# Performance work log

Hardware: AMD Instinct MI355X
Metric: run time of the kernel (lower is better)

The kernel has to match this reference:

```python
import jax, jax.numpy as jnp
import numpy as np
from jax import lax

K = 5          # pooling window (kernel_size=5, padding=2)
PAD = 2
NEG_SLOPE = 0.01  # LeakyReLU default


def _avg_pool5(x):
    # count_include_pad=True (torch default): zero-pad then divide by K
    s = lax.reduce_window(x, 0.0, lax.add, (1, 1, K), (1, 1, 1),
                          ((0, 0), (0, 0), (PAD, PAD)))
    return s / K


def _max_pool5(x):
    return lax.reduce_window(x, -jnp.inf, lax.max, (1, 1, K), (1, 1, 1),
                             ((0, 0), (0, 0), (PAD, PAD)))


def setup_inputs() -> dict:
    key = jax.random.key(0)
    k1, k2, k3 = jax.random.split(key, 3)
    B, C, T = 32, 128, 4096
    x = jax.random.normal(k1, (B, C, T), dtype=jnp.float32)
    conv_weight = jax.random.normal(k2, (C, 1, 6, K), dtype=jnp.float32) * 0.1
    conv_bias = jax.random.normal(k3, (C,), dtype=jnp.float32) * 0.1
    return {"x": x, "conv_weight": conv_weight, "conv_bias": conv_bias}


def reference(x, conv_weight, conv_bias):
    B, C, T = x.shape
    g_mean = jnp.broadcast_to(jnp.mean(x, axis=2, keepdims=True), (B, C, T))
    avg_x = _avg_pool5(x)
    avg_x2 = _avg_pool5(x * x)
    rolling_var = jnp.maximum(avg_x2 - avg_x * avg_x, 1e-6)
    rolling_std = jnp.sqrt(rolling_var)
    third_moment = (x - avg_x) ** 3
    rolling_max = _max_pool5(x)
    rolling_min = -_max_pool5(-x)
    # dropout is identity in eval mode
    gen_in = jnp.stack([x, g_mean, rolling_std, third_moment,
                        rolling_max, rolling_min], axis=2)  # [B,C,6,T]
    out = lax.conv_general_dilated(
        gen_in, conv_weight,
        window_strides=(1, 1),
        padding=((0, 0), (PAD, PAD)),
        dimension_numbers=("NCHW", "OIHW", "NCHW"),
        feature_group_count=C)  # [B,C,1,T]
    out = out + conv_bias[None, :, None, None]
    out = out[:, :, :, :T]
    out = jnp.where(out > 0, out, NEG_SLOPE * out)  # LeakyReLU
    out = jnp.squeeze(out, axis=2)  # [B,C,T]
    return jnp.transpose(x + out, (0, 2, 1))  # [B,T,C]
```

## Files before the change

### kernel.cpp

```cpp
#include <hip/hip_runtime.h>
#include <math.h>

#define T_LEN 4096
#define C_CH  128
#define B_N   32

__global__ __launch_bounds__(256) void row_mean_kernel(const float* __restrict__ x,
                                                       float* __restrict__ means) {
    const int wid  = ((blockIdx.x << 8) + threadIdx.x) >> 6;
    const int lane = threadIdx.x & 63;
    const float4* r = (const float4*)(x + ((size_t)wid << 12));
    float s = 0.f;
    #pragma unroll
    for (int i = 0; i < 16; ++i) {
        float4 v = r[lane + (i << 6)];
        s += (v.x + v.y) + (v.z + v.w);
    }
    #pragma unroll
    for (int off = 32; off > 0; off >>= 1) s += __shfl_down(s, off, 64);
    if (lane == 0) means[wid] = s * (1.0f / T_LEN);
}

#define LT 16
#define TT 64

__global__ __launch_bounds__(256, 4) void fused_kernel(const float* __restrict__ x,
                                                       const float* __restrict__ w,
                                                       const float* __restrict__ bias,
                                                       const float* __restrict__ means,
                                                       float* __restrict__ out) {
    const int b    = blockIdx.z;
    const int cblk = blockIdx.y;
    const int tblk = blockIdx.x;
    const int tid  = threadIdx.x;
    const int c    = cblk * 64 + (tid & 63);
    const int th   = tid >> 6;
    const int ts   = tblk * TT + th * LT;

    const float* xr  = x + ((size_t)(b * C_CH + c)) * T_LEN;
    const float mean = means[b * C_CH + c];
    const float bs   = bias[c];

    float2 wv2[15];
    const float2* pw2 = (const float2*)(w + c * 30);
    #pragma unroll
    for (int i = 0; i < 15; ++i) wv2[i] = pw2[i];
    #define W(idx) (((idx) & 1) ? wv2[(idx) >> 1].y : wv2[(idx) >> 1].x)

    const int gbase = ts - 8;
    float* po = out + ((size_t)(b * T_LEN + ts)) * C_CH + c;

    if (gbase >= 0 && gbase + 32 <= T_LEN) {
        float va[32];
        const float4* p = (const float4*)(xr + gbase);
        #pragma unroll
        for (int i = 0; i < 8; ++i) {
            float4 v = p[i];
            va[4*i+0] = v.x; va[4*i+1] = v.y; va[4*i+2] = v.z; va[4*i+3] = v.w;
        }

        const float w1s = ((W(5) + W(6)) + (W(7) + W(8))) + W(9);
        float acc[LT];
        #pragma unroll
        for (int i = 0; i < LT; ++i) acc[i] = fmaf(mean, w1s, bs);

        #pragma unroll
        for (int lj = 0; lj < LT + 4; ++lj) {
            const float v0 = va[lj+4], v1 = va[lj+5], v2 = va[lj+6], v3 = va[lj+7], v4 = va[lj+8];
            const float s  = ((v0 + v1) + (v2 + v3)) + v4;
            float s2 = v0 * v0;
            s2 = fmaf(v1, v1, s2); s2 = fmaf(v2, v2, s2);
            s2 = fmaf(v3, v3, s2); s2 = fmaf(v4, v4, s2);
            const float mx = fmaxf(fmaxf(fmaxf(v0, v1), fmaxf(v2, v3)), v4);
            const float mn = fminf(fminf(fminf(v0, v1), fminf(v2, v3)), v4);
            const float avg = s * 0.2f;
            float var = fmaf(-avg, avg, s2 * 0.2f);
            var = fmaxf(var, 1e-6f);
            const float sd = __builtin_amdgcn_sqrtf(var);
            const float dm = v2 - avg;
            const float tm = dm * dm * dm;

            #pragma unroll
            for (int dt = -2; dt <= 2; ++dt) {
                const int lt = lj - 2 + dt;
                if (lt < 0 || lt >= LT) continue;
                const int k = 2 - dt;
                float a = acc[lt];
                a = fmaf(v2, W(k),      a);
                a = fmaf(sd, W(10 + k), a);
                a = fmaf(tm, W(15 + k), a);
                a = fmaf(mx, W(20 + k), a);
                a = fmaf(mn, W(25 + k), a);
                acc[lt] = a;
            }
        }

        #pragma unroll
        for (int lt = 0; lt < LT; ++lt) {
            float o = acc[lt];
            o = fmaxf(o, 0.01f * o);
            po[lt * C_CH] = va[lt + 8] + o;
        }
    } else {
        float va[32];
        #pragma unroll
        for (int i = 0; i < 32; ++i) {
            int g = gbase + i;
            va[i] = (g >= 0 && g < T_LEN) ? xr[g] : 0.f;
        }
        float acc[LT];
        #pragma unroll
        for (int i = 0; i < LT; ++i) acc[i] = bs;

        #pragma unroll
        for (int lj = 0; lj < LT + 4; ++lj) {
            const int j = ts - 2 + lj;
            if (j < 0 || j >= T_LEN) continue;
            float s = 0.f, s2 = 0.f, mx = -INFINITY, mn = INFINITY;
            #pragma unroll
            for (int d = -2; d <= 2; ++d) {
                int gk = j + d;
                if (gk >= 0 && gk < T_LEN) {
                    float v = va[lj + 6 + d];
                    s += v; s2 = fmaf(v, v, s2);
                    mx = fmaxf(mx, v); mn = fminf(mn, v);
                }
            }
            const float avg = s * 0.2f;
            float var = fmaf(-avg, avg, s2 * 0.2f);
            var = fmaxf(var, 1e-6f);
            const float sd = __builtin_amdgcn_sqrtf(var);
            const float xc = va[lj + 6];
            const float dm = xc - avg;
            const float tm = dm * dm * dm;

            #pragma unroll
            for (int dt = -2; dt <= 2; ++dt) {
                const int lt = lj - 2 + dt;
                if (lt < 0 || lt >= LT) continue;
                const int k = 2 - dt;
                float a = acc[lt];
                a = fmaf(xc,   W(k),      a);
                a = fmaf(mean, W(5 + k),  a);
                a = fmaf(sd,   W(10 + k), a);
                a = fmaf(tm,   W(15 + k), a);
                a = fmaf(mx,   W(20 + k), a);
                a = fmaf(mn,   W(25 + k), a);
                acc[lt] = a;
            }
        }

        #pragma unroll
        for (int lt = 0; lt < LT; ++lt) {
            float o = acc[lt];
            o = fmaxf(o, 0.01f * o);
            po[lt * C_CH] = va[lt + 8] + o;
        }
    }
    #undef W
}

extern "C" void kernel_launch(void* const* d_in, const int* in_sizes, int n_in,
                              void* d_out, int out_size, void* d_ws, size_t ws_size,
                              hipStream_t stream) {
    const float* x    = (const float*)d_in[0];
    const float* w    = (const float*)d_in[1];
    const float* bias = (const float*)d_in[2];
    float* means = (float*)d_ws;
    float* out   = (float*)d_out;

    row_mean_kernel<<<dim3((B_N * C_CH) / 4), dim3(256), 0, stream>>>(x, means);
    fused_kernel<<<dim3(T_LEN / TT, C_CH / 64, B_N), dim3(256), 0, stream>>>(x, w, bias, means, out);
}
```

Before: 139.0 us.

## Stage x tile with halo in LDS via cooperative float4 loads and transpose

```diff
diff --git a/kernel.cpp b/kernel.cpp
--- a/kernel.cpp
+++ b/kernel.cpp
@@ -4,6 +4,11 @@
 #define T_LEN 4096
 #define C_CH  128
 #define B_N   32
+#define LT 16
+#define TT 64
+#define NT_BLK (T_LEN / TT)
+#define HALO 80
+#define LSTR 65
 
 __global__ __launch_bounds__(256) void row_mean_kernel(const float* __restrict__ x,
                                                        float* __restrict__ means) {
@@ -21,23 +26,44 @@
     if (lane == 0) means[wid] = s * (1.0f / T_LEN);
 }
 
-#define LT 16
-#define TT 64
-
 __global__ __launch_bounds__(256, 4) void fused_kernel(const float* __restrict__ x,
                                                        const float* __restrict__ w,
                                                        const float* __restrict__ bias,
                                                        const float* __restrict__ means,
                                                        float* __restrict__ out) {
+    __shared__ float lds[HALO * LSTR];
     const int b    = blockIdx.z;
     const int cblk = blockIdx.y;
     const int tblk = blockIdx.x;
     const int tid  = threadIdx.x;
-    const int c    = cblk * 64 + (tid & 63);
-    const int th   = tid >> 6;
-    const int ts   = tblk * TT + th * LT;
+    const int T0   = tblk * TT;
+    const float* xc0 = x + ((size_t)b * C_CH + cblk * 64) * T_LEN;
 
-    const float* xr  = x + ((size_t)(b * C_CH + c)) * T_LEN;
+    const bool edge = (tblk == 0) || (tblk == NT_BLK - 1);
+
+    #pragma unroll
+    for (int k = 0; k < 5; ++k) {
+        const int j  = tid + (k << 8);
+        const int r  = j / 20;
+        const int q  = j - r * 20;
+        const int tg = T0 - 8 + (q << 2);
+        float4 v;
+        if (!edge || ((unsigned)tg < (unsigned)T_LEN)) {
+            v = *(const float4*)(xc0 + (size_t)r * T_LEN + tg);
+        } else {
+            v.x = 0.f; v.y = 0.f; v.z = 0.f; v.w = 0.f;
+        }
+        float* dst = &lds[(size_t)(tg - (T0 - 8)) * LSTR + r];
+        dst[0 * LSTR] = v.x; dst[1 * LSTR] = v.y;
+        dst[2 * LSTR] = v.z; dst[3 * LSTR] = v.w;
+    }
+    __syncthreads();
+
+    const int ci = tid & 63;
+    const int th = tid >> 6;
+    const int c  = cblk * 64 + ci;
+    const int ts = T0 + th * LT;
+
     const float mean = means[b * C_CH + c];
     const float bs   = bias[c];
 
@@ -47,18 +73,16 @@
     for (int i = 0; i < 15; ++i) wv2[i] = pw2[i];
     #define W(idx) (((idx) & 1) ? wv2[(idx) >> 1].y : wv2[(idx) >> 1].x)
 
-    const int gbase = ts - 8;
+    float va[32];
+    {
+        const float* src = &lds[(size_t)(th * LT) * LSTR + ci];
+        #pragma unroll
+        for (int i = 0; i < 32; ++i) va[i] = src[i * LSTR];
+    }
+
     float* po = out + ((size_t)(b * T_LEN + ts)) * C_CH + c;
 
-    if (gbase >= 0 && gbase + 32 <= T_LEN) {
-        float va[32];
-        const float4* p = (const float4*)(xr + gbase);
-        #pragma unroll
-        for (int i = 0; i < 8; ++i) {
-            float4 v = p[i];
-            va[4*i+0] = v.x; va[4*i+1] = v.y; va[4*i+2] = v.z; va[4*i+3] = v.w;
-        }
-
+    if (!edge) {
         const float w1s = ((W(5) + W(6)) + (W(7) + W(8))) + W(9);
         float acc[LT];
         #pragma unroll
@@ -102,12 +126,6 @@
             po[lt * C_CH] = va[lt + 8] + o;
         }
     } else {
-        float va[32];
-        #pragma unroll
-        for (int i = 0; i < 32; ++i) {
-            int g = gbase + i;
-            va[i] = (g >= 0 && g < T_LEN) ? xr[g] : 0.f;
-        }
         float acc[LT];
         #pragma unroll
         for (int i = 0; i < LT; ++i) acc[i] = bs;
@@ -170,5 +188,5 @@
     float* out   = (float*)d_out;
 
     row_mean_kernel<<<dim3((B_N * C_CH) / 4), dim3(256), 0, stream>>>(x, means);
-    fused_kernel<<<dim3(T_LEN / TT, C_CH / 64, B_N), dim3(256), 0, stream>>>(x, w, bias, means, out);
+    fused_kernel<<<dim3(NT_BLK, C_CH / 64, B_N), dim3(256), 0, stream>>>(x, w, bias, means, out);
 }
```

New measurement: 190.8 us. 37.3% more time.

## Process four time tiles per block with register prefetch of next window

Applied to the files above, without the earlier changes.

```diff
diff --git a/kernel.cpp b/kernel.cpp
--- a/kernel.cpp
+++ b/kernel.cpp
@@ -4,6 +4,10 @@
 #define T_LEN 4096
 #define C_CH  128
 #define B_N   32
+#define LT 16
+#define TT 64
+#define TILES 4
+#define NT_BLK (T_LEN / (TT * TILES))
 
 __global__ __launch_bounds__(256) void row_mean_kernel(const float* __restrict__ x,
                                                        float* __restrict__ means) {
@@ -21,44 +25,12 @@
     if (lane == 0) means[wid] = s * (1.0f / T_LEN);
 }
 
-#define LT 16
-#define TT 64
-
-__global__ __launch_bounds__(256, 4) void fused_kernel(const float* __restrict__ x,
-                                                       const float* __restrict__ w,
-                                                       const float* __restrict__ bias,
-                                                       const float* __restrict__ means,
-                                                       float* __restrict__ out) {
-    const int b    = blockIdx.z;
-    const int cblk = blockIdx.y;
-    const int tblk = blockIdx.x;
-    const int tid  = threadIdx.x;
-    const int c    = cblk * 64 + (tid & 63);
-    const int th   = tid >> 6;
-    const int ts   = tblk * TT + th * LT;
-
-    const float* xr  = x + ((size_t)(b * C_CH + c)) * T_LEN;
-    const float mean = means[b * C_CH + c];
-    const float bs   = bias[c];
-
-    float2 wv2[15];
-    const float2* pw2 = (const float2*)(w + c * 30);
-    #pragma unroll
-    for (int i = 0; i < 15; ++i) wv2[i] = pw2[i];
-    #define W(idx) (((idx) & 1) ? wv2[(idx) >> 1].y : wv2[(idx) >> 1].x)
-
-    const int gbase = ts - 8;
-    float* po = out + ((size_t)(b * T_LEN + ts)) * C_CH + c;
-
-    if (gbase >= 0 && gbase + 32 <= T_LEN) {
-        float va[32];
-        const float4* p = (const float4*)(xr + gbase);
-        #pragma unroll
-        for (int i = 0; i < 8; ++i) {
-            float4 v = p[i];
-            va[4*i+0] = v.x; va[4*i+1] = v.y; va[4*i+2] = v.z; va[4*i+3] = v.w;
-        }
-
+#define W(idx) (((idx) & 1) ? wv2[(idx) >> 1].y : wv2[(idx) >> 1].x)
+
+__device__ __forceinline__ void compute_store(const float (&va)[32], const float2 (&wv2)[15],
+                                              float mean, float bs, float* __restrict__ po,
+                                              int ts) {
+    if (ts - 8 >= 0 && ts + 24 <= T_LEN) {
         const float w1s = ((W(5) + W(6)) + (W(7) + W(8))) + W(9);
         float acc[LT];
         #pragma unroll
@@ -79,7 +51,6 @@
             const float sd = __builtin_amdgcn_sqrtf(var);
             const float dm = v2 - avg;
             const float tm = dm * dm * dm;
-
             #pragma unroll
             for (int dt = -2; dt <= 2; ++dt) {
                 const int lt = lj - 2 + dt;
@@ -94,7 +65,6 @@
                 acc[lt] = a;
             }
         }
-
         #pragma unroll
         for (int lt = 0; lt < LT; ++lt) {
             float o = acc[lt];
@@ -102,16 +72,9 @@
             po[lt * C_CH] = va[lt + 8] + o;
         }
     } else {
-        float va[32];
-        #pragma unroll
-        for (int i = 0; i < 32; ++i) {
-            int g = gbase + i;
-            va[i] = (g >= 0 && g < T_LEN) ? xr[g] : 0.f;
-        }
         float acc[LT];
         #pragma unroll
         for (int i = 0; i < LT; ++i) acc[i] = bs;
-
         #pragma unroll
         for (int lj = 0; lj < LT + 4; ++lj) {
             const int j = ts - 2 + lj;
@@ -133,7 +96,6 @@
             const float xc = va[lj + 6];
             const float dm = xc - avg;
             const float tm = dm * dm * dm;
-
             #pragma unroll
             for (int dt = -2; dt <= 2; ++dt) {
                 const int lt = lj - 2 + dt;
@@ -149,7 +111,6 @@
                 acc[lt] = a;
             }
         }
-
         #pragma unroll
         for (int lt = 0; lt < LT; ++lt) {
             float o = acc[lt];
@@ -157,7 +118,80 @@
             po[lt * C_CH] = va[lt + 8] + o;
         }
     }
-    #undef W
+}
+
+__device__ __forceinline__ void load_window_guarded(float (&va)[32], const float* __restrict__ xr,
+                                                    int ts) {
+    #pragma unroll
+    for (int i = 0; i < 32; ++i) {
+        int g = ts - 8 + i;
+        va[i] = (g >= 0 && g < T_LEN) ? xr[g] : 0.f;
+    }
+}
+
+__global__ __launch_bounds__(256, 4) void fused_kernel(const float* __restrict__ x,
+                                                       const float* __restrict__ w,
+                                                       const float* __restrict__ bias,
+                                                       const float* __restrict__ means,
+                                                       float* __restrict__ out) {
+    const int b    = blockIdx.z;
+    const int cblk = blockIdx.y;
+    const int tblk = blockIdx.x;
+    const int tid  = threadIdx.x;
+    const int c    = cblk * 64 + (tid & 63);
+    const int th   = tid >> 6;
+    const int Tb   = tblk * (TT * TILES);
+
+    const float* xr  = x + ((size_t)(b * C_CH + c)) * T_LEN;
+    const float mean = means[b * C_CH + c];
+    const float bs   = bias[c];
+
+    float2 wv2[15];
+    const float2* pw2 = (const float2*)(w + c * 30);
+    #pragma unroll
+    for (int i = 0; i < 15; ++i) wv2[i] = pw2[i];
+
+    int ts = Tb + th * LT;
+    float va[32];
+    float4 nb[8];
+
+    if (ts - 8 >= 0 && ts + 24 <= T_LEN) {
+        const float4* p = (const float4*)(xr + ts - 8);
+        #pragma unroll
+        for (int i = 0; i < 8; ++i) {
+            float4 v = p[i];
+            va[4*i+0] = v.x; va[4*i+1] = v.y; va[4*i+2] = v.z; va[4*i+3] = v.w;
+        }
+    } else {
+        load_window_guarded(va, xr, ts);
+    }
+
+    #pragma unroll
+    for (int i = 0; i < TILES; ++i) {
+        const int tsn = ts + TT;
+        const bool can_pref = (i + 1 < TILES) && (tsn - 8 >= 0) && (tsn + 24 <= T_LEN);
+        if (can_pref) {
+            const float4* pn = (const float4*)(xr + tsn - 8);
+            #pragma unroll
+            for (int k = 0; k < 8; ++k) nb[k] = pn[k];
+        }
+
+        float* po = out + ((size_t)(b * T_LEN + ts)) * C_CH + c;
+        compute_store(va, wv2, mean, bs, po, ts);
+
+        if (i + 1 < TILES) {
+            if (can_pref) {
+                #pragma unroll
+                for (int k = 0; k < 8; ++k) {
+                    va[4*k+0] = nb[k].x; va[4*k+1] = nb[k].y;
+                    va[4*k+2] = nb[k].z; va[4*k+3] = nb[k].w;
+                }
+            } else {
+                load_window_guarded(va, xr, tsn);
+            }
+        }
+        ts = tsn;
+    }
 }
 
 extern "C" void kernel_launch(void* const* d_in, const int* in_sizes, int n_in,
@@ -170,5 +204,5 @@
     float* out   = (float*)d_out;
 
     row_mean_kernel<<<dim3((B_N * C_CH) / 4), dim3(256), 0, stream>>>(x, means);
-    fused_kernel<<<dim3(T_LEN / TT, C_CH / 64, B_N), dim3(256), 0, stream>>>(x, w, bias, means, out);
-}
+    fused_kernel<<<dim3(NT_BLK, C_CH / 64, B_N), dim3(256), 0, stream>>>(x, w, bias, means, out);
+}
```

Result: slower. 177.8 us (+27.9%).
